# Optimization experiments

Measured on AMD Instinct MI355X. Metric: run time of the kernel, lower is better.

## Reference

```python
import jax, jax.numpy as jnp
import numpy as np

N = 100000      # nodes
E = 1600000     # edges (avg degree 16)
IN = 128
OUT = 256


def setup_inputs() -> dict:
    key = jax.random.key(0)
    ks = jax.random.split(key, 8)
    x = jax.random.normal(ks[0], (N, IN), dtype=jnp.float32)
    edge_index = jax.random.randint(ks[1], (2, E), 0, N, dtype=jnp.int64)
    # GCNConv weights (glorot-ish scale) and biases
    W1 = jax.random.normal(ks[2], (IN, OUT), dtype=jnp.float32) / np.float32(np.sqrt(IN))
    b1 = jnp.zeros((OUT,), jnp.float32)
    W2 = jax.random.normal(ks[3], (OUT, OUT), dtype=jnp.float32) / np.float32(np.sqrt(OUT))
    b2 = jnp.zeros((OUT,), jnp.float32)
    # projection Linear(IN, OUT)
    Wp = jax.random.normal(ks[4], (IN, OUT), dtype=jnp.float32) / np.float32(np.sqrt(IN))
    bp = jax.random.normal(ks[5], (OUT,), dtype=jnp.float32) * 0.01
    return {"x": x, "edge_index": edge_index, "W1": W1, "b1": b1,
            "W2": W2, "b2": b2, "Wp": Wp, "bp": bp}


def _gcn_conv(x, W, b, src, dst, n):
    """PyG GCNConv: D^{-1/2}(A+I)D^{-1/2} X W + b. src/dst already include self-loops."""
    xw = x @ W                                              # [n, out]
    ones = jnp.ones(src.shape[0], dtype=xw.dtype)
    deg = jax.ops.segment_sum(ones, dst, num_segments=n)    # in-degree incl. self-loop
    dinv = jnp.where(deg > 0, jax.lax.rsqrt(deg), 0.0)
    norm = dinv[src] * dinv[dst]                            # [e]
    msgs = xw[src] * norm[:, None]                          # gather + scale
    out = jax.ops.segment_sum(msgs, dst, num_segments=n)    # scatter-add
    return out + b


def reference(x, edge_index, W1, b1, W2, b2, Wp, bp):
    n = x.shape[0]
    loop = jnp.arange(n, dtype=edge_index.dtype)            # self-loops
    src = jnp.concatenate([edge_index[0], loop])
    dst = jnp.concatenate([edge_index[1], loop])
    out = jax.nn.relu(_gcn_conv(x, W1, b1, src, dst, n))
    out = _gcn_conv(out, W2, b2, src, dst, n)
    identity = x @ Wp + bp                                  # projection (IN != OUT)
    return jax.nn.relu(out + identity)
```

## Files before the change

kernel.cpp:

```cpp
#include <hip/hip_runtime.h>

#define NODES 100000
#define EDGES 1600000
#define FIN   128
#define FOUT  256
#define NBUCK 196

typedef __bf16 bf16;
typedef __bf16 bf16x8 __attribute__((ext_vector_type(8)));
typedef __bf16 bf16x4 __attribute__((ext_vector_type(4)));
typedef __bf16 bf16x2 __attribute__((ext_vector_type(2)));
typedef float  f32x4  __attribute__((ext_vector_type(4)));
typedef float  f32x2  __attribute__((ext_vector_type(2)));

__device__ __forceinline__ f32x2 bf2f(unsigned w) {
    f32x2 r;
    r[0] = __uint_as_float(w << 16);
    r[1] = __uint_as_float(w & 0xffff0000u);
    return r;
}

__device__ __forceinline__ void acc_u4(f32x2 a[4], uint4 w) {
    a[0] += bf2f(w.x); a[1] += bf2f(w.y);
    a[2] += bf2f(w.z); a[3] += bf2f(w.w);
}

__global__ __launch_bounds__(256) void detect_kernel(const void* __restrict__ x,
                                                     const int* __restrict__ ei,
                                                     int* __restrict__ flags,
                                                     float* __restrict__ zpadA,
                                                     float* __restrict__ zpadB) {
    __shared__ int s_f32_evidence;
    __shared__ int s_odd_nonzero;
    int t = threadIdx.x;
    zpadA[t] = 0.0f;
    zpadB[t] = 0.0f;
    if (t == 0) { s_f32_evidence = 0; s_odd_nonzero = 0; }
    __syncthreads();
    const bf16* xb = (const bf16*)x;
    int local_f32 = 0;
    for (int i = t; i < 4096; i += 256) {
        float v = fabsf((float)xb[i]);
        if (!(v < 1e4f)) local_f32 = 1;
    }
    if (local_f32) atomicOr(&s_f32_evidence, 1);
    int local_odd = 0;
    for (int k = t; k < 1024; k += 256) {
        if (ei[2 * k + 1] != 0) local_odd = 1;
    }
    if (local_odd) atomicOr(&s_odd_nonzero, 1);
    __syncthreads();
    if (t == 0) {
        flags[0] = s_f32_evidence ? 0 : 1;
        flags[1] = s_odd_nonzero ? 0 : 1;
    }
}

__device__ __forceinline__ int edge_at(const int* __restrict__ ei, int which, int i,
                                       int is64) {
    if (is64) return ei[2 * (which * EDGES + i)];
    return ei[which * EDGES + i];
}

__global__ __launch_bounds__(512) void deg_count(const int* __restrict__ ei,
                                                 int* __restrict__ deg,
                                                 int* __restrict__ bhist,
                                                 const int* __restrict__ flags) {
    __shared__ int lh[256];
    int t = threadIdx.x;
    if (t < 256) lh[t] = 0;
    __syncthreads();
    int i = blockIdx.x * 512 + t;
    if (i < EDGES) {
        int is64 = flags[1];
        int s = edge_at(ei, 0, i, is64);
        int d = edge_at(ei, 1, i, is64);
        if (s >= 0 && s < NODES && d >= 0 && d < NODES) {
            atomicAdd(&deg[d], 1);
            atomicAdd(&lh[d >> 9], 1);
        }
    }
    __syncthreads();
    if (t < NBUCK && lh[t] > 0) atomicAdd(&bhist[t], lh[t]);
}

__global__ __launch_bounds__(1024) void scan1(const int* __restrict__ deg,
                                              int* __restrict__ col_ptr,
                                              int* __restrict__ blksum, int n) {
    __shared__ int sm[1024];
    int t = threadIdx.x;
    int i = blockIdx.x * 1024 + t;
    int v = (i < n) ? deg[i] + 1 : 0;
    sm[t] = v;
    __syncthreads();
    for (int off = 1; off < 1024; off <<= 1) {
        int u = (t >= off) ? sm[t - off] : 0;
        __syncthreads();
        sm[t] += u;
        __syncthreads();
    }
    if (i <= n) col_ptr[i] = sm[t] - v;
    if (t == 1023) blksum[blockIdx.x] = sm[t];
}

__global__ __launch_bounds__(256) void scan2b(int* __restrict__ blk, int nblk,
                                              const int* __restrict__ bhist,
                                              int* __restrict__ bbase,
                                              int* __restrict__ bcur) {
    __shared__ int sm[256];
    int t = threadIdx.x;
    int v = (t < nblk) ? blk[t] : 0;
    sm[t] = v;
    __syncthreads();
    for (int off = 1; off < 256; off <<= 1) {
        int u = (t >= off) ? sm[t - off] : 0;
        __syncthreads();
        sm[t] += u;
        __syncthreads();
    }
    if (t < nblk) blk[t] = sm[t] - v;
    __syncthreads();
    int v2 = (t < NBUCK) ? bhist[t] : 0;
    sm[t] = v2;
    __syncthreads();
    for (int off = 1; off < 256; off <<= 1) {
        int u = (t >= off) ? sm[t - off] : 0;
        __syncthreads();
        sm[t] += u;
        __syncthreads();
    }
    if (t < NBUCK) {
        int ex = sm[t] - v2;
        bbase[t] = ex;
        bcur[t]  = ex;
        if (t == NBUCK - 1) bbase[NBUCK] = sm[t];
    }
}

__global__ __launch_bounds__(256) void scan3(int* __restrict__ col_ptr,
                                             const int* __restrict__ blkoff,
                                             const int* __restrict__ deg,
                                             float* __restrict__ dinv,
                                             int* __restrict__ col_idx, int n) {
    int i = blockIdx.x * 256 + threadIdx.x;
    if (i <= n) {
        int v = col_ptr[i] + blkoff[i >> 10];
        col_ptr[i] = v;
        if (i < n) col_idx[v] = i;
    }
    if (i < n) dinv[i] = rsqrtf((float)deg[i] + 1.0f);
}

#define EPB 4096
__global__ __launch_bounds__(256) void partition_edges(const int* __restrict__ ei,
                                                       int* __restrict__ bcur,
                                                       uint2* __restrict__ pairs,
                                                       const int* __restrict__ flags) {
    __shared__ int lh[256], sc[256], lst[256], lcu[256], gb[256];
    __shared__ uint2 stage[EPB];
    int t = threadIdx.x;
    int base = blockIdx.x * EPB;
    int is64 = flags[1];

    lh[t] = 0;
    __syncthreads();

    int es[16], ed[16];
#pragma unroll
    for (int j = 0; j < 16; ++j) {
        int i = base + j * 256 + t;
        int s = -1, d = -1;
        if (i < EDGES) {
            s = edge_at(ei, 0, i, is64);
            d = edge_at(ei, 1, i, is64);
            if (s < 0 || s >= NODES || d < 0 || d >= NODES) d = -1;
        }
        es[j] = s; ed[j] = d;
        if (d >= 0) atomicAdd(&lh[d >> 9], 1);
    }
    __syncthreads();
    sc[t] = lh[t];
    __syncthreads();
    for (int off = 1; off < 256; off <<= 1) {
        int u = (t >= off) ? sc[t - off] : 0;
        __syncthreads();
        sc[t] += u;
        __syncthreads();
    }
    int start = sc[t] - lh[t];
    lst[t] = start;
    lcu[t] = start;
    __syncthreads();
#pragma unroll
    for (int j = 0; j < 16; ++j) {
        if (ed[j] >= 0) {
            int p = atomicAdd(&lcu[ed[j] >> 9], 1);
            stage[p] = make_uint2((unsigned)es[j], (unsigned)ed[j]);
        }
    }
    __syncthreads();
    if (t < NBUCK && lh[t] > 0) gb[t] = atomicAdd(&bcur[t], lh[t]);
    __syncthreads();
    int nval = sc[255];
    for (int slot = t; slot < nval; slot += 256) {
        uint2 e = stage[slot];
        int b = (int)(e.y >> 9);
        pairs[(size_t)gb[b] + (slot - lst[b])] = e;
    }
}

__global__ __launch_bounds__(512) void fine_fill(const uint2* __restrict__ pairs,
                                                 const int* __restrict__ bbase,
                                                 const int* __restrict__ col_ptr,
                                                 int* __restrict__ col_idx) {
    __shared__ int lcur[512];
    int b = blockIdx.x;
    int t = threadIdx.x;
    int node = (b << 9) + t;
    lcur[t] = (node < NODES) ? col_ptr[node] + 1 : 0;
    __syncthreads();
    int beg = bbase[b], end = bbase[b + 1];
    for (int i = beg + t; i < end; i += 512) {
        uint2 e = pairs[i];
        int pos = atomicAdd(&lcur[e.y & 511], 1);
        col_idx[pos] = (int)e.x;
    }
}

__global__ __launch_bounds__(256) void pack_all(const void* __restrict__ W1,
                                                const void* __restrict__ W2,
                                                const void* __restrict__ Wp,
                                                const void* __restrict__ b1,
                                                const void* __restrict__ b2,
                                                const void* __restrict__ bp,
                                                bf16* __restrict__ W1p, bf16* __restrict__ W2p,
                                                bf16* __restrict__ Wpp, bf16* __restrict__ b1b,
                                                bf16* __restrict__ b2b, bf16* __restrict__ bpb,
                                                const int* __restrict__ flags) {
    int fl = flags[0];
    int b = blockIdx.x;
    if (b < 512) {
        const void* W; bf16* Wo; int idx;
        if (b < 128)      { W = W1; Wo = W1p; idx = b * 256 + threadIdx.x; }
        else if (b < 384) { W = W2; Wo = W2p; idx = (b - 128) * 256 + threadIdx.x; }
        else              { W = Wp; Wo = Wpp; idx = (b - 384) * 256 + threadIdx.x; }
        int j    = idx & 7;
        int lane = (idx >> 3) & 63;
        int ct   = (idx >> 9) & 15;
        int kt   = idx >> 13;
        int k = kt * 32 + (lane >> 4) * 8 + j;
        int n = ct * 16 + (lane & 15);
        Wo[idx] = fl ? ((const bf16*)W)[k * 256 + n]
                     : (bf16)(((const float*)W)[k * 256 + n]);
    } else {
        const void* bb; bf16* bo;
        if (b == 512)      { bb = b1; bo = b1b; }
        else if (b == 513) { bb = b2; bo = b2b; }
        else               { bb = bp; bo = bpb; }
        int i = threadIdx.x;
        bo[i] = fl ? ((const bf16*)bb)[i] : (bf16)(((const float*)bb)[i]);
    }
}

__global__ __launch_bounds__(256) void gemm_proj(const void* __restrict__ Av,
                                                 const bf16* __restrict__ Wpk,
                                                 const float* __restrict__ dinv,
                                                 const bf16* __restrict__ biasp,
                                                 const bf16* __restrict__ bias2,
                                                 void* __restrict__ outv,
                                                 bf16* __restrict__ Xs,
                                                 const int* __restrict__ flags) {
    int a_f32 = (flags[0] == 0);
    int wave = threadIdx.x >> 6;
    int lane = threadIdx.x & 63;
    int row0 = blockIdx.x * 64;
    int lr = lane & 15;
    int lk = (lane >> 4) * 8;

    int arow[4];
    float di4[4];
#pragma unroll
    for (int rf = 0; rf < 4; ++rf) {
        int r = row0 + rf * 16 + lr;
        arow[rf] = r < NODES ? r : (NODES - 1);
        di4[rf] = dinv[arow[rf]];
    }

    f32x4 acc[4][4];
    f32x4 z = {0.f, 0.f, 0.f, 0.f};
#pragma unroll
    for (int i = 0; i < 4; ++i)
#pragma unroll
        for (int j = 0; j < 4; ++j) acc[i][j] = z;

    for (int kt = 0; kt < 4; ++kt) {
        bf16x8 af[4];
        if (!a_f32) {
            const bf16* Ab = (const bf16*)Av + kt * 32 + lk;
#pragma unroll
            for (int rf = 0; rf < 4; ++rf)
                af[rf] = *(const bf16x8*)(Ab + (size_t)arow[rf] * FIN);
        } else {
            const float* Af = (const float*)Av + kt * 32 + lk;
#pragma unroll
            for (int rf = 0; rf < 4; ++rf) {
                const float* p = Af + (size_t)arow[rf] * FIN;
                f32x4 lo = *(const f32x4*)p;
                f32x4 hi = *(const f32x4*)(p + 4);
                af[rf][0] = (bf16)lo[0]; af[rf][1] = (bf16)lo[1];
                af[rf][2] = (bf16)lo[2]; af[rf][3] = (bf16)lo[3];
                af[rf][4] = (bf16)hi[0]; af[rf][5] = (bf16)hi[1];
                af[rf][6] = (bf16)hi[2]; af[rf][7] = (bf16)hi[3];
            }
        }
#pragma unroll
        for (int rf = 0; rf < 4; ++rf) {
            bf16x8 xsv;
#pragma unroll
            for (int j = 0; j < 8; ++j) xsv[j] = (bf16)(di4[rf] * (float)af[rf][j]);
            *(bf16x8*)(Xs + (size_t)arow[rf] * FIN + kt * 32 + lk) = xsv;
        }
        const bf16* wb = Wpk + ((size_t)(kt * 16 + wave * 4) * 64 + lane) * 8;
        bf16x8 bfv[4];
#pragma unroll
        for (int cf = 0; cf < 4; ++cf)
            bfv[cf] = *(const bf16x8*)(wb + cf * 512);
#pragma unroll
        for (int rf = 0; rf < 4; ++rf)
#pragma unroll
            for (int cf = 0; cf < 4; ++cf)
                acc[rf][cf] = __builtin_amdgcn_mfma_f32_16x16x32_bf16(
                    af[rf], bfv[cf], acc[rf][cf], 0, 0, 0);
    }

    int rb = (lane >> 4) * 4;
#pragma unroll
    for (int rf = 0; rf < 4; ++rf) {
#pragma unroll
        for (int r = 0; r < 4; ++r) {
            int row = row0 + rf * 16 + rb + r;
            if (row >= NODES) continue;
#pragma unroll
            for (int cf = 0; cf < 4; ++cf) {
                int col = wave * 64 + cf * 16 + lr;
                float v = acc[rf][cf][r] + (float)biasp[col] + (float)bias2[col];
                size_t off = (size_t)row * 256 + col;
                if (a_f32) ((float*)outv)[off] = v;
                else       ((bf16*)outv)[off]  = (bf16)v;
            }
        }
    }
}

__device__ __forceinline__ f32x2 sel_reduce4(f32x2 a[4], int rg) {
    f32x2 k0 = (rg & 2) ? a[2] : a[0];
    f32x2 k1 = (rg & 2) ? a[3] : a[1];
    f32x2 s0 = (rg & 2) ? a[0] : a[2];
    f32x2 s1 = (rg & 2) ? a[1] : a[3];
    f32x2 t;
    t[0] = __shfl_xor(s0[0], 32); t[1] = __shfl_xor(s0[1], 32); k0 += t;
    t[0] = __shfl_xor(s1[0], 32); t[1] = __shfl_xor(s1[1], 32); k1 += t;
    f32x2 c = (rg & 1) ? k1 : k0;
    f32x2 s = (rg & 1) ? k0 : k1;
    t[0] = __shfl_xor(s[0], 16); t[1] = __shfl_xor(s[1], 16); c += t;
    return c;
}

#define SMLD 264
__global__ __launch_bounds__(512) void g1conv(const int* __restrict__ col_ptr,
                                              const int* __restrict__ col_idx,
                                              const bf16* __restrict__ Xs,
                                              const float* __restrict__ dinv,
                                              const bf16* __restrict__ W1p,
                                              const bf16* __restrict__ W2p,
                                              const bf16* __restrict__ b1b,
                                              bf16* __restrict__ Y2) {
    __shared__ bf16 sm[64][SMLD];
    int wave = threadIdx.x >> 6;
    int lane = threadIdx.x & 63;
    int row0 = blockIdx.x * 64;
    int li = lane & 15;
    int rg = lane >> 4;

    const char* Xl = (const char*)Xs + li * 16;
    for (int k = 0; k < 8; ++k) {
        int node = row0 + wave * 8 + k;
        int nn = node < NODES ? node : (NODES - 1);
        int beg = col_ptr[nn], end = col_ptr[nn + 1];
        float di = dinv[nn];
        f32x2 a[4];
#pragma unroll
        for (int d = 0; d < 4; ++d) { a[d][0] = 0.f; a[d][1] = 0.f; }
        for (int chunk = beg; chunk < end; chunk += 64) {
            int gpos = chunk + lane;
            int idx = -2;
            if (gpos < end) idx = col_idx[gpos];
            int moff = idx << 8;
            int cnt = end - chunk; if (cnt > 64) cnt = 64;
            int j = 0;
            for (; j + 8 <= cnt; j += 8) {
                int so0 = __shfl(moff, j + rg);
                int so1 = __shfl(moff, j + 4 + rg);
                uint4 w0 = *(const uint4*)(Xl + so0);
                uint4 w1 = *(const uint4*)(Xl + so1);
                acc_u4(a, w0); acc_u4(a, w1);
            }
            for (; j < cnt; j += 4) {
                int so = __shfl(moff, j + rg);
                uint4 w = *(const uint4*)(Xl + so);
                acc_u4(a, w);
            }
        }
        f32x2 s = sel_reduce4(a, rg);
        bf16x2 o;
        o[0] = (bf16)(di * s[0]);
        o[1] = (bf16)(di * s[1]);
        *(bf16x2*)&sm[wave * 8 + k][li * 8 + rg * 2] = o;
    }
    __syncthreads();

    int wr = wave & 1;
    int wc = wave >> 1;
    int lr = li;
    int lk = rg * 8;
    f32x4 acc[2][4];
    f32x4 z = {0.f, 0.f, 0.f, 0.f};
#pragma unroll
    for (int i = 0; i < 2; ++i)
#pragma unroll
        for (int j = 0; j < 4; ++j) acc[i][j] = z;
    for (int kt = 0; kt < 4; ++kt) {
        bf16x8 af[2];
#pragma unroll
        for (int rf = 0; rf < 2; ++rf)
            af[rf] = *(const bf16x8*)&sm[wr * 32 + rf * 16 + lr][kt * 32 + lk];
        const bf16* wb = W1p + ((size_t)(kt * 16 + wc * 4) * 64 + lane) * 8;
        bf16x8 bfv[4];
#pragma unroll
        for (int cf = 0; cf < 4; ++cf)
            bfv[cf] = *(const bf16x8*)(wb + cf * 512);
#pragma unroll
        for (int rf = 0; rf < 2; ++rf)
#pragma unroll
            for (int cf = 0; cf < 4; ++cf)
                acc[rf][cf] = __builtin_amdgcn_mfma_f32_16x16x32_bf16(
                    af[rf], bfv[cf], acc[rf][cf], 0, 0, 0);
    }
    __syncthreads();

    int rb = rg * 4;
#pragma unroll
    for (int rf = 0; rf < 2; ++rf)
#pragma unroll
        for (int r = 0; r < 4; ++r) {
            int row = wr * 32 + rf * 16 + rb + r;
#pragma unroll
            for (int cf = 0; cf < 4; ++cf) {
                int col = wc * 64 + cf * 16 + lr;
                float v = acc[rf][cf][r] + (float)b1b[col];
                sm[row][col] = (bf16)fmaxf(v, 0.0f);
            }
        }
    __syncthreads();

#pragma unroll
    for (int i = 0; i < 2; ++i)
#pragma unroll
        for (int j = 0; j < 4; ++j) acc[i][j] = z;
    for (int kt = 0; kt < 8; ++kt) {
        bf16x8 af[2];
#pragma unroll
        for (int rf = 0; rf < 2; ++rf)
            af[rf] = *(const bf16x8*)&sm[wr * 32 + rf * 16 + lr][kt * 32 + lk];
        const bf16* wb = W2p + ((size_t)(kt * 16 + wc * 4) * 64 + lane) * 8;
        bf16x8 bfv[4];
#pragma unroll
        for (int cf = 0; cf < 4; ++cf)
            bfv[cf] = *(const bf16x8*)(wb + cf * 512);
#pragma unroll
        for (int rf = 0; rf < 2; ++rf)
#pragma unroll
            for (int cf = 0; cf < 4; ++cf)
                acc[rf][cf] = __builtin_amdgcn_mfma_f32_16x16x32_bf16(
                    af[rf], bfv[cf], acc[rf][cf], 0, 0, 0);
    }
#pragma unroll
    for (int rf = 0; rf < 2; ++rf)
#pragma unroll
        for (int r = 0; r < 4; ++r) {
            int row = row0 + wr * 32 + rf * 16 + rb + r;
            if (row >= NODES) continue;
            float di = dinv[row];
#pragma unroll
            for (int cf = 0; cf < 4; ++cf) {
                int col = wc * 64 + cf * 16 + lr;
                Y2[(size_t)row * 256 + col] = (bf16)(acc[rf][cf][r] * di);
            }
        }
}

__global__ __launch_bounds__(256) void gather2(const int* __restrict__ col_ptr,
                                               const int* __restrict__ col_idx,
                                               const bf16* __restrict__ Y2,
                                               const float* __restrict__ dinv,
                                               void* __restrict__ outv,
                                               const int* __restrict__ flags) {
    int io_f32 = (flags[0] == 0);
    int b = blockIdx.x;
    int slice = b & 1;
    int wave  = threadIdx.x >> 6;
    int wid   = (b >> 1) * 4 + wave;
    int lane  = threadIdx.x & 63;
    if (wid >= NODES) return;
    int beg = col_ptr[wid], end = col_ptr[wid + 1];
    int li = lane & 15;
    int rg = lane >> 4;
    int ch0 = slice * 128 + li * 8 + rg * 2;
    size_t obase = (size_t)wid * 256 + ch0;

    float di = dinv[wid];
    float pj0, pj1;
    if (io_f32) {
        f32x2 p = *(const f32x2*)((const float*)outv + obase);
        pj0 = p[0]; pj1 = p[1];
    } else {
        bf16x2 p = *(const bf16x2*)((const bf16*)outv + obase);
        pj0 = (float)p[0]; pj1 = (float)p[1];
    }

    const char* Yl = (const char*)Y2 + slice * 256 + li * 16;
    f32x2 acc2[4];
#pragma unroll
    for (int d = 0; d < 4; ++d) { acc2[d][0] = 0.f; acc2[d][1] = 0.f; }
    for (int chunk = beg; chunk < end; chunk += 64) {
        int gpos = chunk + lane;
        int idx = -2;
        if (gpos < end) idx = col_idx[gpos];
        int moff = idx << 9;
        int cnt = end - chunk; if (cnt > 64) cnt = 64;
        int j = 0;
        for (; j + 16 <= cnt; j += 16) {
            int so0 = __shfl(moff, j + rg);
            int so1 = __shfl(moff, j + 4 + rg);
            int so2 = __shfl(moff, j + 8 + rg);
            int so3 = __shfl(moff, j + 12 + rg);
            uint4 w0 = *(const uint4*)(Yl + so0);
            uint4 w1 = *(const uint4*)(Yl + so1);
            uint4 w2 = *(const uint4*)(Yl + so2);
            uint4 w3 = *(const uint4*)(Yl + so3);
            acc_u4(acc2, w0); acc_u4(acc2, w1);
            acc_u4(acc2, w2); acc_u4(acc2, w3);
        }
        for (; j < cnt; j += 4) {
            int so = __shfl(moff, j + rg);
            uint4 w = *(const uint4*)(Yl + so);
            acc_u4(acc2, w);
        }
    }
    f32x2 s = sel_reduce4(acc2, rg);
    float r0 = fmaxf(di * s[0] + pj0, 0.0f);
    float r1 = fmaxf(di * s[1] + pj1, 0.0f);

    if (io_f32) {
        f32x2 o; o[0] = r0; o[1] = r1;
        __builtin_nontemporal_store(o, (f32x2*)((float*)outv + obase));
    } else {
        bf16x2 o; o[0] = (bf16)r0; o[1] = (bf16)r1;
        __builtin_nontemporal_store(o, (bf16x2*)((bf16*)outv + obase));
    }
}

__global__ __launch_bounds__(256) void zero_out(bf16* out, int nelem) {
    int i = blockIdx.x * 256 + threadIdx.x;
    if (i < nelem) out[i] = (bf16)0.0f;
}

extern "C" void kernel_launch(void* const* d_in, const int* in_sizes, int n_in,
                              void* d_out, int out_size, void* d_ws, size_t ws_size,
                              hipStream_t stream) {
    const void* x   = d_in[0];
    const int*  ei  = (const int*)d_in[1];
    const void* W1  = d_in[2];
    const void* b1  = d_in[3];
    const void* W2  = d_in[4];
    const void* b2  = d_in[5];
    const void* Wp  = d_in[6];
    const void* bp  = d_in[7];

    const size_t CIDX_ALLOC = 6800384;
    const size_t NEEDED = 85075456;
    if (ws_size < NEEDED) {
        zero_out<<<(NODES * 256 + 255) / 256, 256, 0, stream>>>((bf16*)d_out, NODES * 256);
        return;
    }

    char* w = (char*)d_ws;
    int*   col_ptr = (int*)w;   w += 401408;
    int*   deg     = (int*)w;   w += 401408;
    int*   bhist   = (int*)w;   w += 1024;
    float* dinv    = (float*)w; w += 401408;
    int*   blk     = (int*)w;   w += 1024;
    int*   flags   = (int*)w;   w += 1024;
    int*   bbase   = (int*)w;   w += 1024;
    int*   bcur    = (int*)w;   w += 1024;
    int*   col_idx = (int*)w;   w += CIDX_ALLOC;
    bf16*  W1p     = (bf16*)w;  w += 65536;
    bf16*  W2p     = (bf16*)w;  w += 131072;
    bf16*  Wpp     = (bf16*)w;  w += 65536;
    bf16*  b1b     = (bf16*)w;  w += 512;
    bf16*  b2b     = (bf16*)w;  w += 512;
    bf16*  bpb     = (bf16*)w;  w += 512;
    char*  zpadA   = w;         w += 1024;
    bf16*  Xs      = (bf16*)w;  w += 25600000;
    char*  zpadB   = w;         w += 1024;
    bf16*  Y2      = (bf16*)w;  w += 51200000;
    uint2* pairs   = (uint2*)Xs;

    const int NBLK = (NODES + 1 + 1023) / 1024;

    detect_kernel<<<1, 256, 0, stream>>>(x, ei, flags, (float*)zpadA, (float*)zpadB);

    hipMemsetAsync(deg, 0, 401408 + 1024, stream);
    deg_count<<<(EDGES + 511) / 512, 512, 0, stream>>>(ei, deg, bhist, flags);

    scan1<<<NBLK, 1024, 0, stream>>>(deg, col_ptr, blk, NODES);
    scan2b<<<1, 256, 0, stream>>>(blk, NBLK, bhist, bbase, bcur);
    scan3<<<(NODES + 256) / 256, 256, 0, stream>>>(col_ptr, blk, deg, dinv, col_idx, NODES);

    partition_edges<<<(EDGES + EPB - 1) / EPB, 256, 0, stream>>>(ei, bcur, pairs, flags);
    fine_fill<<<NBUCK, 512, 0, stream>>>(pairs, bbase, col_ptr, col_idx);

    pack_all<<<515, 256, 0, stream>>>(W1, W2, Wp, b1, b2, bp,
                                      W1p, W2p, Wpp, b1b, b2b, bpb, flags);

    const int gemm_grid = (NODES + 63) / 64;
    const int g2_grid   = ((NODES + 3) / 4) * 2;

    gemm_proj<<<gemm_grid, 256, 0, stream>>>(x, Wpp, dinv, bpb, b2b, d_out, Xs, flags);
    g1conv<<<gemm_grid, 512, 0, stream>>>(col_ptr, col_idx, Xs, dinv,
                                          W1p, W2p, b1b, Y2);
    gather2<<<g2_grid, 256, 0, stream>>>(col_ptr, col_idx, Y2, dinv, d_out, flags);
}
```

Before: 594.5 us.

## Merge preprocessing kernels into fewer launches and stash projection in bf16 buffer

Cuts the launch count by folding kernels together. The memset goes into an init kernel, the weight packing joins degree counting, the block scans are recomputed inside the partition and scan3 kernel, and fine_fill now shares a launch with the projection GEMM. Pairs move into the Y2 buffer so the CSR fill and the Xs-writing GEMM can run concurrently. When the workspace is large enough, the fp32 projection result is written to a separate bf16 buffer instead of the output, which halves that intermediate traffic at some precision cost. The price is redundant small scans in every block and heterogeneous blocks sharing one launch.

```diff
diff --git a/kernel.cpp b/kernel.cpp
--- a/kernel.cpp
+++ b/kernel.cpp
@@ -5,6 +5,7 @@
 #define FIN   128
 #define FOUT  256
 #define NBUCK 196
+#define NBLKS 98
 
 typedef __bf16 bf16;
 typedef __bf16 bf16x8 __attribute__((ext_vector_type(8)));
@@ -25,16 +26,28 @@
     a[2] += bf2f(w.z); a[3] += bf2f(w.w);
 }
 
-__global__ __launch_bounds__(256) void detect_kernel(const void* __restrict__ x,
-                                                     const int* __restrict__ ei,
-                                                     int* __restrict__ flags,
-                                                     float* __restrict__ zpadA,
-                                                     float* __restrict__ zpadB) {
+__device__ __forceinline__ int edge_at(const int* __restrict__ ei, int which, int i,
+                                       int is64) {
+    if (is64) return ei[2 * (which * EDGES + i)];
+    return ei[which * EDGES + i];
+}
+
+__global__ __launch_bounds__(256) void init_kernel(const void* __restrict__ x,
+                                                   const int* __restrict__ ei,
+                                                   int* __restrict__ zero0,
+                                                   int* __restrict__ flags,
+                                                   float* __restrict__ zpadA,
+                                                   float* __restrict__ zpadB) {
+    int b = blockIdx.x, t = threadIdx.x;
+    if (b < 394) {
+        int i = b * 256 + t;
+        if (i < 100864) zero0[i] = 0;
+        return;
+    }
+    zpadA[t] = 0.0f;
+    zpadB[t] = 0.0f;
     __shared__ int s_f32_evidence;
     __shared__ int s_odd_nonzero;
-    int t = threadIdx.x;
-    zpadA[t] = 0.0f;
-    zpadB[t] = 0.0f;
     if (t == 0) { s_f32_evidence = 0; s_odd_nonzero = 0; }
     __syncthreads();
     const bf16* xb = (const bf16*)x;
@@ -56,189 +69,41 @@
     }
 }
 
-__device__ __forceinline__ int edge_at(const int* __restrict__ ei, int which, int i,
-                                       int is64) {
-    if (is64) return ei[2 * (which * EDGES + i)];
-    return ei[which * EDGES + i];
-}
-
-__global__ __launch_bounds__(512) void deg_count(const int* __restrict__ ei,
-                                                 int* __restrict__ deg,
-                                                 int* __restrict__ bhist,
-                                                 const int* __restrict__ flags) {
-    __shared__ int lh[256];
-    int t = threadIdx.x;
-    if (t < 256) lh[t] = 0;
-    __syncthreads();
-    int i = blockIdx.x * 512 + t;
-    if (i < EDGES) {
-        int is64 = flags[1];
-        int s = edge_at(ei, 0, i, is64);
-        int d = edge_at(ei, 1, i, is64);
-        if (s >= 0 && s < NODES && d >= 0 && d < NODES) {
-            atomicAdd(&deg[d], 1);
-            atomicAdd(&lh[d >> 9], 1);
-        }
-    }
-    __syncthreads();
-    if (t < NBUCK && lh[t] > 0) atomicAdd(&bhist[t], lh[t]);
-}
-
-__global__ __launch_bounds__(1024) void scan1(const int* __restrict__ deg,
-                                              int* __restrict__ col_ptr,
-                                              int* __restrict__ blksum, int n) {
-    __shared__ int sm[1024];
-    int t = threadIdx.x;
-    int i = blockIdx.x * 1024 + t;
-    int v = (i < n) ? deg[i] + 1 : 0;
-    sm[t] = v;
-    __syncthreads();
-    for (int off = 1; off < 1024; off <<= 1) {
-        int u = (t >= off) ? sm[t - off] : 0;
-        __syncthreads();
-        sm[t] += u;
-        __syncthreads();
-    }
-    if (i <= n) col_ptr[i] = sm[t] - v;
-    if (t == 1023) blksum[blockIdx.x] = sm[t];
-}
-
-__global__ __launch_bounds__(256) void scan2b(int* __restrict__ blk, int nblk,
-                                              const int* __restrict__ bhist,
-                                              int* __restrict__ bbase,
-                                              int* __restrict__ bcur) {
-    __shared__ int sm[256];
-    int t = threadIdx.x;
-    int v = (t < nblk) ? blk[t] : 0;
-    sm[t] = v;
-    __syncthreads();
-    for (int off = 1; off < 256; off <<= 1) {
-        int u = (t >= off) ? sm[t - off] : 0;
-        __syncthreads();
-        sm[t] += u;
-        __syncthreads();
-    }
-    if (t < nblk) blk[t] = sm[t] - v;
-    __syncthreads();
-    int v2 = (t < NBUCK) ? bhist[t] : 0;
-    sm[t] = v2;
-    __syncthreads();
-    for (int off = 1; off < 256; off <<= 1) {
-        int u = (t >= off) ? sm[t - off] : 0;
-        __syncthreads();
-        sm[t] += u;
-        __syncthreads();
-    }
-    if (t < NBUCK) {
-        int ex = sm[t] - v2;
-        bbase[t] = ex;
-        bcur[t]  = ex;
-        if (t == NBUCK - 1) bbase[NBUCK] = sm[t];
-    }
-}
-
-__global__ __launch_bounds__(256) void scan3(int* __restrict__ col_ptr,
-                                             const int* __restrict__ blkoff,
-                                             const int* __restrict__ deg,
-                                             float* __restrict__ dinv,
-                                             int* __restrict__ col_idx, int n) {
-    int i = blockIdx.x * 256 + threadIdx.x;
-    if (i <= n) {
-        int v = col_ptr[i] + blkoff[i >> 10];
-        col_ptr[i] = v;
-        if (i < n) col_idx[v] = i;
-    }
-    if (i < n) dinv[i] = rsqrtf((float)deg[i] + 1.0f);
-}
-
-#define EPB 4096
-__global__ __launch_bounds__(256) void partition_edges(const int* __restrict__ ei,
-                                                       int* __restrict__ bcur,
-                                                       uint2* __restrict__ pairs,
-                                                       const int* __restrict__ flags) {
-    __shared__ int lh[256], sc[256], lst[256], lcu[256], gb[256];
-    __shared__ uint2 stage[EPB];
-    int t = threadIdx.x;
-    int base = blockIdx.x * EPB;
-    int is64 = flags[1];
-
-    lh[t] = 0;
-    __syncthreads();
-
-    int es[16], ed[16];
-#pragma unroll
-    for (int j = 0; j < 16; ++j) {
-        int i = base + j * 256 + t;
-        int s = -1, d = -1;
+__global__ __launch_bounds__(512) void degcnt_pack(const int* __restrict__ ei,
+                                                   int* __restrict__ deg,
+                                                   int* __restrict__ bhist,
+                                                   const void* __restrict__ W1,
+                                                   const void* __restrict__ W2,
+                                                   const void* __restrict__ Wp,
+                                                   const void* __restrict__ b1,
+                                                   const void* __restrict__ b2,
+                                                   const void* __restrict__ bp,
+                                                   bf16* __restrict__ W1p, bf16* __restrict__ W2p,
+                                                   bf16* __restrict__ Wpp, bf16* __restrict__ b1b,
+                                                   bf16* __restrict__ b2b, bf16* __restrict__ bpb,
+                                                   const int* __restrict__ flags) {
+    if (blockIdx.x < 3125) {
+        __shared__ int lh[256];
+        int t = threadIdx.x;
+        if (t < 256) lh[t] = 0;
+        __syncthreads();
+        int i = blockIdx.x * 512 + t;
         if (i < EDGES) {
-            s = edge_at(ei, 0, i, is64);
-            d = edge_at(ei, 1, i, is64);
-            if (s < 0 || s >= NODES || d < 0 || d >= NODES) d = -1;
-        }
-        es[j] = s; ed[j] = d;
-        if (d >= 0) atomicAdd(&lh[d >> 9], 1);
-    }
-    __syncthreads();
-    sc[t] = lh[t];
-    __syncthreads();
-    for (int off = 1; off < 256; off <<= 1) {
-        int u = (t >= off) ? sc[t - off] : 0;
-        __syncthreads();
-        sc[t] += u;
-        __syncthreads();
-    }
-    int start = sc[t] - lh[t];
-    lst[t] = start;
-    lcu[t] = start;
-    __syncthreads();
-#pragma unroll
-    for (int j = 0; j < 16; ++j) {
-        if (ed[j] >= 0) {
-            int p = atomicAdd(&lcu[ed[j] >> 9], 1);
-            stage[p] = make_uint2((unsigned)es[j], (unsigned)ed[j]);
-        }
-    }
-    __syncthreads();
-    if (t < NBUCK && lh[t] > 0) gb[t] = atomicAdd(&bcur[t], lh[t]);
-    __syncthreads();
-    int nval = sc[255];
-    for (int slot = t; slot < nval; slot += 256) {
-        uint2 e = stage[slot];
-        int b = (int)(e.y >> 9);
-        pairs[(size_t)gb[b] + (slot - lst[b])] = e;
-    }
-}
-
-__global__ __launch_bounds__(512) void fine_fill(const uint2* __restrict__ pairs,
-                                                 const int* __restrict__ bbase,
-                                                 const int* __restrict__ col_ptr,
-                                                 int* __restrict__ col_idx) {
-    __shared__ int lcur[512];
-    int b = blockIdx.x;
-    int t = threadIdx.x;
-    int node = (b << 9) + t;
-    lcur[t] = (node < NODES) ? col_ptr[node] + 1 : 0;
-    __syncthreads();
-    int beg = bbase[b], end = bbase[b + 1];
-    for (int i = beg + t; i < end; i += 512) {
-        uint2 e = pairs[i];
-        int pos = atomicAdd(&lcur[e.y & 511], 1);
-        col_idx[pos] = (int)e.x;
-    }
-}
-
-__global__ __launch_bounds__(256) void pack_all(const void* __restrict__ W1,
-                                                const void* __restrict__ W2,
-                                                const void* __restrict__ Wp,
-                                                const void* __restrict__ b1,
-                                                const void* __restrict__ b2,
-                                                const void* __restrict__ bp,
-                                                bf16* __restrict__ W1p, bf16* __restrict__ W2p,
-                                                bf16* __restrict__ Wpp, bf16* __restrict__ b1b,
-                                                bf16* __restrict__ b2b, bf16* __restrict__ bpb,
-                                                const int* __restrict__ flags) {
+            int is64 = flags[1];
+            int s = edge_at(ei, 0, i, is64);
+            int d = edge_at(ei, 1, i, is64);
+            if (s >= 0 && s < NODES && d >= 0 && d < NODES) {
+                atomicAdd(&deg[d], 1);
+                atomicAdd(&lh[d >> 9], 1);
+            }
+        }
+        __syncthreads();
+        if (t < NBUCK && lh[t] > 0) atomicAdd(&bhist[t], lh[t]);
+        return;
+    }
+    if (threadIdx.x >= 256) return;
     int fl = flags[0];
-    int b = blockIdx.x;
+    int b = blockIdx.x - 3125;
     if (b < 512) {
         const void* W; bf16* Wo; int idx;
         if (b < 128)      { W = W1; Wo = W1p; idx = b * 256 + threadIdx.x; }
@@ -262,18 +127,169 @@
     }
 }
 
-__global__ __launch_bounds__(256) void gemm_proj(const void* __restrict__ Av,
-                                                 const bf16* __restrict__ Wpk,
-                                                 const float* __restrict__ dinv,
-                                                 const bf16* __restrict__ biasp,
-                                                 const bf16* __restrict__ bias2,
-                                                 void* __restrict__ outv,
-                                                 bf16* __restrict__ Xs,
-                                                 const int* __restrict__ flags) {
+__global__ __launch_bounds__(1024) void scan1(const int* __restrict__ deg,
+                                              int* __restrict__ col_ptr,
+                                              int* __restrict__ blksum, int n) {
+    __shared__ int sm[1024];
+    int t = threadIdx.x;
+    int i = blockIdx.x * 1024 + t;
+    int v = (i < n) ? deg[i] + 1 : 0;
+    sm[t] = v;
+    __syncthreads();
+    for (int off = 1; off < 1024; off <<= 1) {
+        int u = (t >= off) ? sm[t - off] : 0;
+        __syncthreads();
+        sm[t] += u;
+        __syncthreads();
+    }
+    if (i <= n) col_ptr[i] = sm[t] - v;
+    if (t == 1023) blksum[blockIdx.x] = sm[t];
+}
+
+#define EPB 4096
+__global__ __launch_bounds__(256) void part_scan3(const int* __restrict__ ei,
+                                                  const int* __restrict__ bhist,
+                                                  int* __restrict__ bcur,
+                                                  uint2* __restrict__ pairs,
+                                                  const int* __restrict__ flags,
+                                                  int* __restrict__ col_ptr,
+                                                  const int* __restrict__ blk,
+                                                  const int* __restrict__ deg,
+                                                  float* __restrict__ dinv,
+                                                  int* __restrict__ col_idx, int n) {
+    if (blockIdx.x < 391) {
+        __shared__ int lh[256], sc[256], lst[256], lcu[256], gb[256], bs[256];
+        __shared__ uint2 stage[EPB];
+        int t = threadIdx.x;
+        int base = blockIdx.x * EPB;
+        int is64 = flags[1];
+
+        lh[t] = 0;
+        __syncthreads();
+
+        int es[16], ed[16];
+#pragma unroll
+        for (int j = 0; j < 16; ++j) {
+            int i = base + j * 256 + t;
+            int s = -1, d = -1;
+            if (i < EDGES) {
+                s = edge_at(ei, 0, i, is64);
+                d = edge_at(ei, 1, i, is64);
+                if (s < 0 || s >= NODES || d < 0 || d >= NODES) d = -1;
+            }
+            es[j] = s; ed[j] = d;
+            if (d >= 0) atomicAdd(&lh[d >> 9], 1);
+        }
+        __syncthreads();
+        sc[t] = lh[t];
+        __syncthreads();
+        for (int off = 1; off < 256; off <<= 1) {
+            int u = (t >= off) ? sc[t - off] : 0;
+            __syncthreads();
+            sc[t] += u;
+            __syncthreads();
+        }
+        int start = sc[t] - lh[t];
+        lst[t] = start;
+        lcu[t] = start;
+        __syncthreads();
+#pragma unroll
+        for (int j = 0; j < 16; ++j) {
+            if (ed[j] >= 0) {
+                int p = atomicAdd(&lcu[ed[j] >> 9], 1);
+                stage[p] = make_uint2((unsigned)es[j], (unsigned)ed[j]);
+            }
+        }
+        __syncthreads();
+        int v2 = (t < NBUCK) ? bhist[t] : 0;
+        bs[t] = v2;
+        __syncthreads();
+        for (int off = 1; off < 256; off <<= 1) {
+            int u = (t >= off) ? bs[t - off] : 0;
+            __syncthreads();
+            bs[t] += u;
+            __syncthreads();
+        }
+        if (t < NBUCK && lh[t] > 0)
+            gb[t] = (bs[t] - v2) + atomicAdd(&bcur[t], lh[t]);
+        __syncthreads();
+        int nval = sc[255];
+        for (int slot = t; slot < nval; slot += 256) {
+            uint2 e = stage[slot];
+            int b = (int)(e.y >> 9);
+            pairs[(size_t)gb[b] + (slot - lst[b])] = e;
+        }
+        return;
+    }
+    __shared__ int sb[128];
+    int t = threadIdx.x;
+    int sid = blockIdx.x - 391;
+    int ov = 0;
+    if (t < 128) { ov = (t < NBLKS) ? blk[t] : 0; sb[t] = ov; }
+    __syncthreads();
+    for (int off = 1; off < 128; off <<= 1) {
+        int u = (t >= off && t < 128) ? sb[t - off] : 0;
+        __syncthreads();
+        if (t < 128) sb[t] += u;
+        __syncthreads();
+    }
+    if (t < 128) sb[t] -= ov;
+    __syncthreads();
+    int i = sid * 256 + t;
+    if (i <= n) {
+        int v = col_ptr[i] + sb[i >> 10];
+        col_ptr[i] = v;
+        if (i < n) col_idx[v] = i;
+    }
+    if (i < n) dinv[i] = rsqrtf((float)deg[i] + 1.0f);
+}
+
+__global__ __launch_bounds__(256) void ff_proj(const uint2* __restrict__ pairs,
+                                               const int* __restrict__ bhist,
+                                               const int* __restrict__ col_ptr,
+                                               int* __restrict__ col_idx,
+                                               const void* __restrict__ Av,
+                                               const bf16* __restrict__ Wpk,
+                                               const float* __restrict__ dinv,
+                                               const bf16* __restrict__ biasp,
+                                               const bf16* __restrict__ bias2,
+                                               void* __restrict__ outv,
+                                               bf16* __restrict__ projb,
+                                               int use_projb,
+                                               bf16* __restrict__ Xs,
+                                               const int* __restrict__ flags) {
+    if (blockIdx.x < NBUCK) {
+        __shared__ int lcur[512];
+        __shared__ int bs2[256];
+        int b = blockIdx.x;
+        int t = threadIdx.x;
+        int v2 = (t < NBUCK) ? bhist[t] : 0;
+        bs2[t] = v2;
+        __syncthreads();
+        for (int off = 1; off < 256; off <<= 1) {
+            int u = (t >= off) ? bs2[t - off] : 0;
+            __syncthreads();
+            bs2[t] += u;
+            __syncthreads();
+        }
+        int be = bs2[b];
+        int bb = be - bhist[b];
+        int node = (b << 9) + t;
+        lcur[t] = (node < NODES) ? col_ptr[node] + 1 : 0;
+        int node2 = node + 256;
+        lcur[t + 256] = (node2 < NODES) ? col_ptr[node2] + 1 : 0;
+        __syncthreads();
+        for (int i = bb + t; i < be; i += 256) {
+            uint2 e = pairs[i];
+            int pos = atomicAdd(&lcur[e.y & 511], 1);
+            col_idx[pos] = (int)e.x;
+        }
+        return;
+    }
     int a_f32 = (flags[0] == 0);
     int wave = threadIdx.x >> 6;
     int lane = threadIdx.x & 63;
-    int row0 = blockIdx.x * 64;
+    int row0 = (blockIdx.x - NBUCK) * 64;
     int lr = lane & 15;
     int lk = (lane >> 4) * 8;
 
@@ -345,8 +361,12 @@
                 int col = wave * 64 + cf * 16 + lr;
                 float v = acc[rf][cf][r] + (float)biasp[col] + (float)bias2[col];
                 size_t off = (size_t)row * 256 + col;
-                if (a_f32) ((float*)outv)[off] = v;
-                else       ((bf16*)outv)[off]  = (bf16)v;
+                if (a_f32) {
+                    if (use_projb) projb[off] = (bf16)v;
+                    else           ((float*)outv)[off] = v;
+                } else {
+                    ((bf16*)outv)[off] = (bf16)v;
+                }
             }
         }
     }
@@ -503,6 +523,8 @@
                                                const int* __restrict__ col_idx,
                                                const bf16* __restrict__ Y2,
                                                const float* __restrict__ dinv,
+                                               const bf16* __restrict__ projb,
+                                               int use_projb,
                                                void* __restrict__ outv,
                                                const int* __restrict__ flags) {
     int io_f32 = (flags[0] == 0);
@@ -521,8 +543,13 @@
     float di = dinv[wid];
     float pj0, pj1;
     if (io_f32) {
-        f32x2 p = *(const f32x2*)((const float*)outv + obase);
-        pj0 = p[0]; pj1 = p[1];
+        if (use_projb) {
+            bf16x2 p = *(const bf16x2*)(projb + obase);
+            pj0 = (float)p[0]; pj1 = (float)p[1];
+        } else {
+            f32x2 p = *(const f32x2*)((const float*)outv + obase);
+            pj0 = p[0]; pj1 = p[1];
+        }
     } else {
         bf16x2 p = *(const bf16x2*)((const bf16*)outv + obase);
         pj0 = (float)p[0]; pj1 = (float)p[1];
@@ -588,21 +615,22 @@
     const void* bp  = d_in[7];
 
     const size_t CIDX_ALLOC = 6800384;
-    const size_t NEEDED = 85075456;
+    const size_t NEEDED     = 85074432;
+    const size_t NEEDED_BIG = NEEDED + 51200000;
     if (ws_size < NEEDED) {
         zero_out<<<(NODES * 256 + 255) / 256, 256, 0, stream>>>((bf16*)d_out, NODES * 256);
         return;
     }
+    int use_projb = (ws_size >= NEEDED_BIG) ? 1 : 0;
 
     char* w = (char*)d_ws;
     int*   col_ptr = (int*)w;   w += 401408;
     int*   deg     = (int*)w;   w += 401408;
     int*   bhist   = (int*)w;   w += 1024;
+    int*   bcur    = (int*)w;   w += 1024;
     float* dinv    = (float*)w; w += 401408;
     int*   blk     = (int*)w;   w += 1024;
     int*   flags   = (int*)w;   w += 1024;
-    int*   bbase   = (int*)w;   w += 1024;
-    int*   bcur    = (int*)w;   w += 1024;
     int*   col_idx = (int*)w;   w += CIDX_ALLOC;
     bf16*  W1p     = (bf16*)w;  w += 65536;
     bf16*  W2p     = (bf16*)w;  w += 131072;
@@ -614,30 +642,26 @@
     bf16*  Xs      = (bf16*)w;  w += 25600000;
     char*  zpadB   = w;         w += 1024;
     bf16*  Y2      = (bf16*)w;  w += 51200000;
-    uint2* pairs   = (uint2*)Xs;
-
-    const int NBLK = (NODES + 1 + 1023) / 1024;
-
-    detect_kernel<<<1, 256, 0, stream>>>(x, ei, flags, (float*)zpadA, (float*)zpadB);
-
-    hipMemsetAsync(deg, 0, 401408 + 1024, stream);
-    deg_count<<<(EDGES + 511) / 512, 512, 0, stream>>>(ei, deg, bhist, flags);
-
-    scan1<<<NBLK, 1024, 0, stream>>>(deg, col_ptr, blk, NODES);
-    scan2b<<<1, 256, 0, stream>>>(blk, NBLK, bhist, bbase, bcur);
-    scan3<<<(NODES + 256) / 256, 256, 0, stream>>>(col_ptr, blk, deg, dinv, col_idx, NODES);
-
-    partition_edges<<<(EDGES + EPB - 1) / EPB, 256, 0, stream>>>(ei, bcur, pairs, flags);
-    fine_fill<<<NBUCK, 512, 0, stream>>>(pairs, bbase, col_ptr, col_idx);
-
-    pack_all<<<515, 256, 0, stream>>>(W1, W2, Wp, b1, b2, bp,
-                                      W1p, W2p, Wpp, b1b, b2b, bpb, flags);
-
-    const int gemm_grid = (NODES + 63) / 64;
-    const int g2_grid   = ((NODES + 3) / 4) * 2;
-
-    gemm_proj<<<gemm_grid, 256, 0, stream>>>(x, Wpp, dinv, bpb, b2b, d_out, Xs, flags);
-    g1conv<<<gemm_grid, 512, 0, stream>>>(col_ptr, col_idx, Xs, dinv,
-                                          W1p, W2p, b1b, Y2);
-    gather2<<<g2_grid, 256, 0, stream>>>(col_ptr, col_idx, Y2, dinv, d_out, flags);
-}
+    bf16*  projb   = (bf16*)w;
+    uint2* pairs   = (uint2*)Y2;
+
+    init_kernel<<<395, 256, 0, stream>>>(x, ei, deg, flags, (float*)zpadA, (float*)zpadB);
+
+    degcnt_pack<<<3640, 512, 0, stream>>>(ei, deg, bhist, W1, W2, Wp, b1, b2, bp,
+                                          W1p, W2p, Wpp, b1b, b2b, bpb, flags);
+
+    scan1<<<NBLKS, 1024, 0, stream>>>(deg, col_ptr, blk, NODES);
+
+    part_scan3<<<391 + 392, 256, 0, stream>>>(ei, bhist, bcur, pairs, flags,
+                                              col_ptr, blk, deg, dinv, col_idx, NODES);
+
+    ff_proj<<<NBUCK + (NODES + 63) / 64, 256, 0, stream>>>(
+        pairs, bhist, col_ptr, col_idx,
+        x, Wpp, dinv, bpb, b2b, d_out, projb, use_projb, Xs, flags);
+
+    g1conv<<<(NODES + 63) / 64, 512, 0, stream>>>(col_ptr, col_idx, Xs, dinv,
+                                                  W1p, W2p, b1b, Y2);
+
+    gather2<<<((NODES + 3) / 4) * 2, 256, 0, stream>>>(col_ptr, col_idx, Y2, dinv,
+                                                       projb, use_projb, d_out, flags);
+}
```

After: 574.9 us. -3.3%, faster.
